# Optimization experiments

Measured on AMD Instinct MI355X. Metric: run time of the kernel, lower is better.

## Reference

```python
import jax, jax.numpy as jnp
import numpy as np

N, E = 50000, 800000
F_NODE, F_EDGE, HID, EMB, HEADS = 128, 16, 64, 32, 4
BN_EPS = 1e-5


def _glorot(key, shape):
    fan_in = shape[0] if len(shape) > 1 else shape[-1]
    return jax.random.normal(key, shape, jnp.float32) / np.sqrt(fan_in)


def setup_inputs() -> dict:
    key = jax.random.key(0)
    ks = jax.random.split(key, 32)
    inp = {
        "x": jax.random.normal(ks[0], (N, F_NODE), jnp.float32),
        "edge_attr": jax.random.normal(ks[1], (E, F_EDGE), jnp.float32),
        # GAT layer 0: in=F_NODE, heads=4, C=HID
        "W0": _glorot(ks[2], (F_NODE, HEADS * HID)),
        "We0": _glorot(ks[3], (F_EDGE, HEADS * HID)),
        "as0": _glorot(ks[4], (HEADS, HID)),
        "ad0": _glorot(ks[5], (HEADS, HID)),
        "ae0": _glorot(ks[6], (HEADS, HID)),
        "b0": jnp.zeros((HEADS * HID,), jnp.float32),
        "bn0_g": jnp.ones((HEADS * HID,), jnp.float32),
        "bn0_b": jnp.zeros((HEADS * HID,), jnp.float32),
        # GAT layer 1: in=HEADS*HID, heads=1, C=EMB
        "W1": _glorot(ks[7], (HEADS * HID, EMB)),
        "We1": _glorot(ks[8], (F_EDGE, EMB)),
        "as1": _glorot(ks[9], (1, EMB)),
        "ad1": _glorot(ks[10], (1, EMB)),
        "ae1": _glorot(ks[11], (1, EMB)),
        "b1": jnp.zeros((EMB,), jnp.float32),
        # node decoder: 32 -> 128 -> 64 -> 128
        "ndW1": _glorot(ks[12], (EMB, 2 * HID)),   "ndb1": jnp.zeros((2 * HID,), jnp.float32),
        "nd_g": jnp.ones((2 * HID,), jnp.float32), "nd_b": jnp.zeros((2 * HID,), jnp.float32),
        "ndW2": _glorot(ks[13], (2 * HID, HID)),   "ndb2": jnp.zeros((HID,), jnp.float32),
        "ndW3": _glorot(ks[14], (HID, F_NODE)),    "ndb3": jnp.zeros((F_NODE,), jnp.float32),
        # edge decoder: 2*32+16=80 -> 128 -> 64 -> 1
        "edW1": _glorot(ks[15], (2 * EMB + F_EDGE, 2 * HID)), "edb1": jnp.zeros((2 * HID,), jnp.float32),
        "ed_g": jnp.ones((2 * HID,), jnp.float32), "ed_b": jnp.zeros((2 * HID,), jnp.float32),
        "edW2": _glorot(ks[16], (2 * HID, HID)),   "edb2": jnp.zeros((HID,), jnp.float32),
        "edW3": _glorot(ks[17], (HID, 1)),         "edb3": jnp.zeros((1,), jnp.float32),
        "edge_index": jax.random.randint(ks[18], (2, E), 0, N, jnp.int64),
    }
    return inp


def _bn(x, g, b):
    # eval-mode BatchNorm1d with running mean 0, var 1
    return x / np.sqrt(1.0 + BN_EPS) * g + b


def _gat(x, edge_index, edge_attr, W, b, We, att_s, att_d, att_e, heads, C):
    n = x.shape[0]
    src, dst = edge_index[0], edge_index[1]
    e = edge_attr.shape[0]
    # add self loops; self-loop edge_attr = scatter-mean of incoming edge_attr (PyG fill_value='mean')
    esum = jax.ops.segment_sum(edge_attr, dst, num_segments=n)
    cnt = jax.ops.segment_sum(jnp.ones((e,), edge_attr.dtype), dst, num_segments=n)
    loop_attr = esum / jnp.maximum(cnt, 1.0)[:, None]
    loop = jnp.arange(n, dtype=src.dtype)
    src_f = jnp.concatenate([src, loop])
    dst_f = jnp.concatenate([dst, loop])
    ea = jnp.concatenate([edge_attr, loop_attr], axis=0)
    xw = (x @ W).reshape(n, heads, C)                       # [N,H,C]
    a_s = (xw * att_s).sum(-1)                              # [N,H]
    a_d = (xw * att_d).sum(-1)
    a_e = ((ea @ We).reshape(-1, heads, C) * att_e).sum(-1)  # [E+N,H]
    alpha = jax.nn.leaky_relu(a_s[src_f] + a_d[dst_f] + a_e, 0.2)
    # segment softmax over destination neighborhoods
    m = jax.ops.segment_max(alpha, dst_f, num_segments=n)
    alpha = jnp.exp(alpha - m[dst_f])
    s = jax.ops.segment_sum(alpha, dst_f, num_segments=n)
    alpha = alpha / (s[dst_f] + 1e-16)
    out = jax.ops.segment_sum(alpha[:, :, None] * xw[src_f], dst_f, num_segments=n)
    return out.reshape(n, heads * C) + b


def reference(x, edge_attr, W0, b0, We0, as0, ad0, ae0, bn0_g, bn0_b,
              W1, b1, We1, as1, ad1, ae1,
              ndW1, ndb1, nd_g, nd_b, ndW2, ndb2, ndW3, ndb3,
              edW1, edb1, ed_g, ed_b, edW2, edb2, edW3, edb3,
              edge_index):
    # encoder
    h = _gat(x, edge_index, edge_attr, W0, b0, We0, as0, ad0, ae0, HEADS, HID)
    h = jax.nn.elu(_bn(h, bn0_g, bn0_b))  # residual skipped: 256 != 128; dropout is eval-mode identity
    z = _gat(h, edge_index, edge_attr, W1, b1, We1, as1, ad1, ae1, 1, EMB)
    # node decoder
    n1 = _bn(jax.nn.relu(z @ ndW1 + ndb1), nd_g, nd_b)
    node_recon = jax.nn.relu(n1 @ ndW2 + ndb2) @ ndW3 + ndb3
    # edge decoder
    src, dst = edge_index[0], edge_index[1]
    ef = jnp.concatenate([z[src], z[dst], edge_attr], axis=1)  # [E, 2*EMB+F_EDGE]
    e1 = _bn(jax.nn.relu(ef @ edW1 + edb1), ed_g, ed_b)
    edge_recon = jax.nn.sigmoid((jax.nn.relu(e1 @ edW2 + edb2) @ edW3 + edb3)).squeeze(-1)
    return (z, node_recon, edge_recon)
```

## Files before the change

### kernel.cpp

```cpp
#include <hip/hip_runtime.h>
#include <math.h>

#define BN_K 0.9999950000374997f

static __device__ __forceinline__ float lrelu02(float x) { return x > 0.f ? x : 0.2f * x; }

typedef _Float16 half8 __attribute__((ext_vector_type(8)));
typedef __fp16 fp16x2 __attribute__((ext_vector_type(2)));
typedef float f32x4 __attribute__((ext_vector_type(4)));

static __device__ __forceinline__ unsigned short f2h(float x)
{
    union { _Float16 h; unsigned short u; } q;
    q.h = (_Float16)x;
    return q.u;
}
static __device__ __forceinline__ float h2f(unsigned short u)
{
    union { unsigned short u; _Float16 h; } q;
    q.u = u;
    return (float)q.h;
}
static __device__ __forceinline__ unsigned pkrtz(float a, float b)
{
    union { fp16x2 h; unsigned u; } q;
    q.h = __builtin_amdgcn_cvt_pkrtz(a, b);
    return q.u;
}

__global__ void k_ae_vec(const float* __restrict__ We0, const float* __restrict__ ae0,
                         const float* __restrict__ We1, const float* __restrict__ ae1,
                         const float* __restrict__ edbb, const float* __restrict__ edW2,
                         const float* __restrict__ edb2,
                         float* __restrict__ v0, float* __restrict__ v1,
                         float* __restrict__ b2p)
{
    int t = threadIdx.x;
    if (t < 64) {
        int h = t >> 4, k = t & 15;
        float s = 0.f;
        for (int c = 0; c < 64; ++c) s += We0[k * 256 + h * 64 + c] * ae0[h * 64 + c];
        v0[h * 16 + k] = s;
    } else if (t < 80) {
        int k = t - 64;
        float s = 0.f;
        for (int c = 0; c < 32; ++c) s += We1[k * 32 + c] * ae1[c];
        v1[k] = s;
    } else if (t < 144) {
        int n = t - 80;
        float s = 0.f;
        for (int k = 0; k < 128; ++k) s += edbb[k] * edW2[k * 64 + n];
        b2p[n] = edb2[n] + s;
    }
}

__global__ void k_deg_init(int* __restrict__ deg, int N)
{
    int i = blockIdx.x * blockDim.x + threadIdx.x;
    if (i < N) deg[i] = 1;
}

__global__ void k_deg_count(const int* __restrict__ dst, int* __restrict__ deg, int E)
{
    int e = blockIdx.x * blockDim.x + threadIdx.x;
    if (e < E) atomicAdd(&deg[dst[e]], 1);
}

#define SCHUNK 4096
__global__ __launch_bounds__(1024) void k_scan1(const int* __restrict__ deg,
                                                int* __restrict__ rowptr,
                                                int* __restrict__ bsum, int n)
{
    __shared__ int sbuf[1024];
    int b = blockIdx.x, t = threadIdx.x;
    int i0 = b * SCHUNK + t * 4;
    int v[4];
#pragma unroll
    for (int j = 0; j < 4; ++j) v[j] = (i0 + j < n) ? deg[i0 + j] : 0;
    int s = v[0] + v[1] + v[2] + v[3];
    sbuf[t] = s;
    __syncthreads();
    for (int d = 1; d < 1024; d <<= 1) {
        int tmp = (t >= d) ? sbuf[t - d] : 0;
        __syncthreads();
        sbuf[t] += tmp;
        __syncthreads();
    }
    int run = sbuf[t] - s;
#pragma unroll
    for (int j = 0; j < 4; ++j) {
        run += v[j];
        if (i0 + j < n) rowptr[i0 + j + 1] = run;
    }
    if (t == 1023) bsum[b] = sbuf[1023];
    if (b == 0 && t == 0) rowptr[0] = 0;
}

__global__ void k_scan3(const int* __restrict__ bsum, const int* __restrict__ deg,
                        int* __restrict__ rowptr, int* __restrict__ cur, int n)
{
    int i = blockIdx.x * blockDim.x + threadIdx.x;
    if (i >= n) return;
    int chunk = i / SCHUNK;
    int off = 0;
    for (int b = 0; b < chunk; ++b) off += bsum[b];
    int r = rowptr[i + 1] + off;
    rowptr[i + 1] = r;
    cur[i] = r - deg[i];
}

__global__ void k_fill(const int* __restrict__ dst, int* __restrict__ cur,
                       int* __restrict__ col, int E, int N)
{
    int t = blockIdx.x * blockDim.x + threadIdx.x;
    if (t >= E + N) return;
    int d = (t < E) ? dst[t] : (t - E);
    int slot = atomicAdd(&cur[d], 1);
    col[slot] = t;
}

__global__ __launch_bounds__(256) void k_loop_mean(
    const int* __restrict__ rowptr, const int* __restrict__ col,
    const float* __restrict__ ea, const float* __restrict__ v0, const float* __restrict__ v1,
    float* __restrict__ a_e0, float* __restrict__ a_e1, int N, int E)
{
    int wv = threadIdx.x >> 6, lane = threadIdx.x & 63;
    int i = blockIdx.x * 4 + wv;
    if (i >= N) return;
    int beg = rowptr[i], end = rowptr[i + 1];
    int q = lane >> 4, k = lane & 15;
    float sum = 0.f;
    for (int p = beg + q; p < end; p += 4) {
        int eid = col[p];
        if (eid < E) sum += ea[(size_t)eid * 16 + k];
    }
    sum += __shfl_xor(sum, 16);
    sum += __shfl_xor(sum, 32);
    int cnt = end - beg - 1;
    float mean = sum / (float)max(cnt, 1);
    float p0 = mean * v0[q * 16 + k];
    float p1 = mean * v1[k];
#pragma unroll
    for (int mm = 1; mm < 16; mm <<= 1) { p0 += __shfl_xor(p0, mm); p1 += __shfl_xor(p1, mm); }
    if (k == 0) a_e0[(size_t)(E + i) * 4 + q] = p0;
    if (lane == 0) a_e1[E + i] = p1;
}

__global__ void k_edge_ae(const float* __restrict__ ea,
                          const float* __restrict__ v0, const float* __restrict__ v1,
                          float* __restrict__ a_e0, float* __restrict__ a_e1,
                          unsigned short* __restrict__ ea16, int E)
{
    int idx = blockIdx.x * blockDim.x + threadIdx.x;
    if (idx >= E) return;
    const float* row = ea + (size_t)idx * 16;
    float r[16];
#pragma unroll
    for (int k = 0; k < 16; ++k) r[k] = row[k];
#pragma unroll
    for (int h = 0; h < 4; ++h) {
        float s = 0.f;
#pragma unroll
        for (int k = 0; k < 16; ++k) s = fmaf(r[k], v0[h * 16 + k], s);
        a_e0[(size_t)idx * 4 + h] = s;
    }
    float s1 = 0.f;
#pragma unroll
    for (int k = 0; k < 16; ++k) s1 = fmaf(r[k], v1[k], s1);
    a_e1[idx] = s1;
#pragma unroll
    for (int k = 0; k < 16; k += 4) {
        ushort4 o;
        o.x = f2h(r[k]); o.y = f2h(r[k + 1]); o.z = f2h(r[k + 2]); o.w = f2h(r[k + 3]);
        *(ushort4*)(ea16 + (size_t)idx * 16 + k) = o;
    }
}

__global__ __launch_bounds__(512) void k_pack_all(
    const float* __restrict__ W0, const float* __restrict__ W1,
    const float* __restrict__ nd1, const float* __restrict__ nd2, const float* __restrict__ nd3,
    const float* __restrict__ ed1, const float* __restrict__ ed2,
    const float* __restrict__ edb1, const float* __restrict__ edg,
    unsigned short* __restrict__ pw)
{
    int f = blockIdx.x, t = threadIdx.x;
    int l = t >> 3, i = t & 7, g = l >> 4, m = l & 15;
    float v;
    if (f < 64) {
        int q = f; int k = 32 * (q >> 4) + 8 * g + i, n = 16 * (q & 15) + m;
        v = W0[(size_t)k * 256 + n];
    } else if (f < 80) {
        int q = f - 64; int k = 32 * (q >> 1) + 8 * g + i, n = 16 * (q & 1) + m;
        v = W1[(size_t)k * 32 + n];
    } else if (f < 88) {
        int q = f - 80; int k = 8 * g + i, n = 16 * q + m;
        v = nd1[(size_t)k * 128 + n];
    } else if (f < 104) {
        int q = f - 88; int k = 32 * (q >> 2) + 8 * g + i, n = 16 * (q & 3) + m;
        v = nd2[(size_t)k * 64 + n];
    } else if (f < 120) {
        int q = f - 104; int k = 32 * (q >> 3) + 8 * g + i, n = 16 * (q & 7) + m;
        v = nd3[(size_t)k * 128 + n];
    } else if (f < 144) {
        int q = f - 120; int k = 32 * (q >> 3) + 8 * g + i, n = 16 * (q & 7) + m;
        v = (k < 80) ? ed1[(size_t)k * 128 + n] : (k == 80 ? edb1[n] : 0.f);
    } else {
        int q = f - 144; int k = 32 * (q >> 2) + 8 * g + i, n = 16 * (q & 3) + m;
        v = ed2[(size_t)k * 64 + n] * (edg[k] * BN_K);
    }
    pw[(size_t)f * 512 + t] = f2h(v);
}

template <int KC, int NT, int MODE, int AF32, int NTOT, int DOTS>
__global__ __launch_bounds__(256) void k_gemm16(
    const void* __restrict__ Ain, const unsigned short* __restrict__ pwB,
    void* __restrict__ outp, int M,
    const float* __restrict__ bias, const float* __restrict__ g_,
    const float* __restrict__ bb_,
    const float* __restrict__ attS, const float* __restrict__ attD,
    float* __restrict__ a_sO, float* __restrict__ a_dO)
{
    constexpr int K = KC * 32;
    constexpr int LDA = K + 8;
    __shared__ unsigned short s_pw[KC * NT * 512];
    __shared__ unsigned short s_a[64 * LDA];
    __shared__ float s_c[3 * NT * 16];

    int t = threadIdx.x;
    int ttoff = blockIdx.y * NT;
    for (int idx = t; idx < KC * NT * 64; idx += 256) {
        int f = idx >> 6, e8 = idx & 63;
        int c = f / NT, tt = f - c * NT;
        *(half8*)&s_pw[(size_t)idx * 8] =
            *(const half8*)&pwB[(((size_t)(c * NTOT + ttoff + tt)) * 64 + e8) * 8];
    }
    if (MODE) {
        for (int c = t; c < NT * 16; c += 256) {
            s_c[c] = bias[ttoff * 16 + c];
            if (MODE == 2) {
                s_c[NT * 16 + c] = g_[ttoff * 16 + c] * BN_K;
                s_c[2 * NT * 16 + c] = bb_[ttoff * 16 + c];
            }
        }
    }
    int wv = t >> 6, lane = t & 63, gq = lane >> 4, m = lane & 15;

    float asv[NT], adv[NT];
    if (DOTS) {
#pragma unroll
        for (int tt = 0; tt < NT; ++tt) {
            asv[tt] = attS[ttoff * 16 + 16 * tt + m];
            adv[tt] = attD[ttoff * 16 + 16 * tt + m];
        }
    }

    int nrt = (M + 63) >> 6;
    for (int rt = blockIdx.x; rt < nrt; rt += gridDim.x) {
        int r0 = rt << 6;
        __syncthreads();
        for (int idx = t; idx < 64 * (K / 8); idx += 256) {
            int row = idx / (K / 8), cb = idx % (K / 8);
            half8 v = {};
            if (r0 + row < M) {
                if (AF32) {
                    const float* Af = (const float*)Ain + (size_t)(r0 + row) * K + cb * 8;
                    float4 u0 = *(const float4*)Af;
                    float4 u1 = *(const float4*)(Af + 4);
                    union { half8 h; unsigned u[4]; } q;
                    q.u[0] = pkrtz(u0.x, u0.y); q.u[1] = pkrtz(u0.z, u0.w);
                    q.u[2] = pkrtz(u1.x, u1.y); q.u[3] = pkrtz(u1.z, u1.w);
                    v = q.h;
                } else {
                    v = *(const half8*)&((const unsigned short*)Ain)[(size_t)(r0 + row) * K + cb * 8];
                }
            }
            *(half8*)&s_a[row * LDA + cb * 8] = v;
        }
        __syncthreads();
        f32x4 acc[NT] = {};
#pragma unroll
        for (int c = 0; c < KC; ++c) {
            half8 a = *(half8*)&s_a[(wv * 16 + m) * LDA + 32 * c + 8 * gq];
#pragma unroll
            for (int tt = 0; tt < NT; ++tt) {
                half8 b = *(const half8*)&s_pw[(c * NT + tt) * 512 + lane * 8];
                acc[tt] = __builtin_amdgcn_mfma_f32_16x16x32_f16(a, b, acc[tt], 0, 0, 0);
            }
        }
#pragma unroll
        for (int tt = 0; tt < NT; ++tt) {
            int col = 16 * tt + m;
            int ocol = ttoff * 16 + col;
            float cb = MODE ? s_c[col] : 0.f;
#pragma unroll
            for (int r = 0; r < 4; ++r) {
                int row = r0 + wv * 16 + 4 * gq + r;
                float v = acc[tt][r] + cb;
                if (MODE == 1) v = fmaxf(v, 0.f);
                if (MODE == 2) v = fmaxf(v, 0.f) * s_c[NT * 16 + col] + s_c[2 * NT * 16 + col];
                if (MODE == 3) {
                    if (row < M) ((float*)outp)[(size_t)row * (NTOT * 16) + ocol] = v;
                } else {
                    float o = __shfl_xor(v, 1);
                    if (!(m & 1) && row < M)
                        *(unsigned*)&((unsigned short*)outp)[(size_t)row * (NTOT * 16) + ocol] =
                            pkrtz(v, o);
                }
            }
        }
        if (DOTS == 1) {
#pragma unroll
            for (int r = 0; r < 4; ++r) {
                float psA = 0.f, pdA = 0.f, psB = 0.f, pdB = 0.f;
#pragma unroll
                for (int tt = 0; tt < NT && tt < 4; ++tt) {
                    psA = fmaf(acc[tt][r], asv[tt], psA);
                    pdA = fmaf(acc[tt][r], adv[tt], pdA);
                }
#pragma unroll
                for (int tt = 4; tt < NT; ++tt) {
                    psB = fmaf(acc[tt][r], asv[tt], psB);
                    pdB = fmaf(acc[tt][r], adv[tt], pdB);
                }
#pragma unroll
                for (int mm = 1; mm < 16; mm <<= 1) {
                    psA += __shfl_xor(psA, mm); pdA += __shfl_xor(pdA, mm);
                    psB += __shfl_xor(psB, mm); pdB += __shfl_xor(pdB, mm);
                }
                int row = r0 + wv * 16 + 4 * gq + r;
                if (m == 0 && row < M) {
                    int hA = 2 * blockIdx.y;
                    a_sO[(size_t)row * 4 + hA] = psA; a_sO[(size_t)row * 4 + hA + 1] = psB;
                    a_dO[(size_t)row * 4 + hA] = pdA; a_dO[(size_t)row * 4 + hA + 1] = pdB;
                }
            }
        } else if (DOTS == 2) {
#pragma unroll
            for (int r = 0; r < 4; ++r) {
                float ps = 0.f, pd = 0.f;
#pragma unroll
                for (int tt = 0; tt < NT; ++tt) {
                    ps = fmaf(acc[tt][r], asv[tt], ps);
                    pd = fmaf(acc[tt][r], adv[tt], pd);
                }
#pragma unroll
                for (int mm = 1; mm < 16; mm <<= 1) {
                    ps += __shfl_xor(ps, mm); pd += __shfl_xor(pd, mm);
                }
                int row = r0 + wv * 16 + 4 * gq + r;
                if (m == 0 && row < M) { a_sO[row] = ps; a_dO[row] = pd; }
            }
        }
    }
}

__global__ __launch_bounds__(64) void k_gat0_agg(
    const int* __restrict__ rowptr, const int* __restrict__ col, const int* __restrict__ srcA,
    const float* __restrict__ a_s, const float* __restrict__ a_d, const float* __restrict__ a_e,
    const unsigned short* __restrict__ xw16, const float* __restrict__ b0,
    const float* __restrict__ bng, const float* __restrict__ bnb,
    unsigned short* __restrict__ hout16, int N, int E)
{
    int i = blockIdx.x;
    int lane = threadIdx.x;
    int beg = rowptr[i], end = rowptr[i + 1];
    float ad[4];
#pragma unroll
    for (int h = 0; h < 4; ++h) ad[h] = a_d[(size_t)i * 4 + h];

    float al[4] = {-1e30f, -1e30f, -1e30f, -1e30f};
    int sl0 = i;
    int p0 = beg + lane;
    if (p0 < end) {
        int eid = col[p0];
        sl0 = (eid < E) ? srcA[eid] : i;
        float4 as4 = *(const float4*)(a_s + (size_t)sl0 * 4);
        float4 ae4 = *(const float4*)(a_e + (size_t)eid * 4);
        al[0] = lrelu02(as4.x + ad[0] + ae4.x);
        al[1] = lrelu02(as4.y + ad[1] + ae4.y);
        al[2] = lrelu02(as4.z + ad[2] + ae4.z);
        al[3] = lrelu02(as4.w + ad[3] + ae4.w);
    }
    float mx[4] = {al[0], al[1], al[2], al[3]};
    for (int p = p0 + 64; p < end; p += 64) {
        int eid = col[p];
        int s = (eid < E) ? srcA[eid] : i;
        float4 as4 = *(const float4*)(a_s + (size_t)s * 4);
        float4 ae4 = *(const float4*)(a_e + (size_t)eid * 4);
        mx[0] = fmaxf(mx[0], lrelu02(as4.x + ad[0] + ae4.x));
        mx[1] = fmaxf(mx[1], lrelu02(as4.y + ad[1] + ae4.y));
        mx[2] = fmaxf(mx[2], lrelu02(as4.z + ad[2] + ae4.z));
        mx[3] = fmaxf(mx[3], lrelu02(as4.w + ad[3] + ae4.w));
    }
#pragma unroll
    for (int h = 0; h < 4; ++h)
#pragma unroll
        for (int m = 1; m < 64; m <<= 1) mx[h] = fmaxf(mx[h], __shfl_xor(mx[h], m));

    __shared__ float wls[256];
    __shared__ int s_src[64];
    int hl = lane >> 4;
    float accx = 0.f, accy = 0.f, accz = 0.f, accw = 0.f;
    float s0 = 0.f, s1 = 0.f, s2 = 0.f, s3 = 0.f;
    for (int base = beg; base < end; base += 64) {
        int p = base + lane;
        int cnt = min(64, end - base);
        if (p < end) {
            float aa0, aa1, aa2, aa3;
            int s;
            if (base == beg) {
                s = sl0;
                aa0 = al[0]; aa1 = al[1]; aa2 = al[2]; aa3 = al[3];
            } else {
                int eid = col[p];
                s = (eid < E) ? srcA[eid] : i;
                float4 as4 = *(const float4*)(a_s + (size_t)s * 4);
                float4 ae4 = *(const float4*)(a_e + (size_t)eid * 4);
                aa0 = lrelu02(as4.x + ad[0] + ae4.x);
                aa1 = lrelu02(as4.y + ad[1] + ae4.y);
                aa2 = lrelu02(as4.z + ad[2] + ae4.z);
                aa3 = lrelu02(as4.w + ad[3] + ae4.w);
            }
            float w0 = expf(aa0 - mx[0]);
            float w1 = expf(aa1 - mx[1]);
            float w2 = expf(aa2 - mx[2]);
            float w3 = expf(aa3 - mx[3]);
            s0 += w0; s1 += w1; s2 += w2; s3 += w3;
            wls[lane * 4 + 0] = w0; wls[lane * 4 + 1] = w1;
            wls[lane * 4 + 2] = w2; wls[lane * 4 + 3] = w3;
            s_src[lane] = s;
        }
        __syncthreads();
        int q = 0;
        for (; q + 3 < cnt; q += 4) {
            int ss0 = s_src[q], ss1 = s_src[q + 1], ss2 = s_src[q + 2], ss3 = s_src[q + 3];
            ushort4 x0 = *(const ushort4*)(xw16 + (size_t)ss0 * 256 + lane * 4);
            ushort4 x1 = *(const ushort4*)(xw16 + (size_t)ss1 * 256 + lane * 4);
            ushort4 x2 = *(const ushort4*)(xw16 + (size_t)ss2 * 256 + lane * 4);
            ushort4 x3 = *(const ushort4*)(xw16 + (size_t)ss3 * 256 + lane * 4);
            float w0 = wls[q * 4 + hl], w1 = wls[(q + 1) * 4 + hl];
            float w2 = wls[(q + 2) * 4 + hl], w3 = wls[(q + 3) * 4 + hl];
            accx = fmaf(w0, h2f(x0.x), accx); accy = fmaf(w0, h2f(x0.y), accy);
            accz = fmaf(w0, h2f(x0.z), accz); accw = fmaf(w0, h2f(x0.w), accw);
            accx = fmaf(w1, h2f(x1.x), accx); accy = fmaf(w1, h2f(x1.y), accy);
            accz = fmaf(w1, h2f(x1.z), accz); accw = fmaf(w1, h2f(x1.w), accw);
            accx = fmaf(w2, h2f(x2.x), accx); accy = fmaf(w2, h2f(x2.y), accy);
            accz = fmaf(w2, h2f(x2.z), accz); accw = fmaf(w2, h2f(x2.w), accw);
            accx = fmaf(w3, h2f(x3.x), accx); accy = fmaf(w3, h2f(x3.y), accy);
            accz = fmaf(w3, h2f(x3.z), accz); accw = fmaf(w3, h2f(x3.w), accw);
        }
        for (; q < cnt; ++q) {
            int ss = s_src[q];
            float w = wls[q * 4 + hl];
            ushort4 xv = *(const ushort4*)(xw16 + (size_t)ss * 256 + lane * 4);
            accx = fmaf(w, h2f(xv.x), accx);
            accy = fmaf(w, h2f(xv.y), accy);
            accz = fmaf(w, h2f(xv.z), accz);
            accw = fmaf(w, h2f(xv.w), accw);
        }
        __syncthreads();
    }
#pragma unroll
    for (int m = 1; m < 64; m <<= 1) {
        s0 += __shfl_xor(s0, m); s1 += __shfl_xor(s1, m);
        s2 += __shfl_xor(s2, m); s3 += __shfl_xor(s3, m);
    }
    float sden = ((hl == 0) ? s0 : (hl == 1) ? s1 : (hl == 2) ? s2 : s3) + 1e-16f;

    int ch = lane * 4;
    float out[4] = {accx / sden, accy / sden, accz / sden, accw / sden};
    ushort4 ov;
    unsigned short* po = (unsigned short*)&ov;
#pragma unroll
    for (int j = 0; j < 4; ++j) {
        int c = ch + j;
        float v = out[j] + b0[c];
        v = v * (BN_K * bng[c]) + bnb[c];
        po[j] = f2h((v > 0.f) ? v : expm1f(v));
    }
    *(ushort4*)(hout16 + (size_t)i * 256 + ch) = ov;
}

__global__ __launch_bounds__(64) void k_gat1_agg(
    const int* __restrict__ rowptr, const int* __restrict__ col, const int* __restrict__ srcA,
    const float* __restrict__ a_s, const float* __restrict__ a_d, const float* __restrict__ a_e,
    const unsigned short* __restrict__ xw16, const float* __restrict__ b1,
    float* __restrict__ zout, unsigned short* __restrict__ z16, int N, int E)
{
    int i = blockIdx.x;
    int lane = threadIdx.x;
    int beg = rowptr[i], end = rowptr[i + 1];
    float ad = a_d[i];
    float al = -1e30f;
    int sl0 = i;
    int p0 = beg + lane;
    if (p0 < end) {
        int eid = col[p0];
        sl0 = (eid < E) ? srcA[eid] : i;
        al = lrelu02(a_s[sl0] + ad + a_e[eid]);
    }
    float mx = al;
    for (int p = p0 + 64; p < end; p += 64) {
        int eid = col[p];
        int s = (eid < E) ? srcA[eid] : i;
        mx = fmaxf(mx, lrelu02(a_s[s] + ad + a_e[eid]));
    }
#pragma unroll
    for (int m = 1; m < 64; m <<= 1) mx = fmaxf(mx, __shfl_xor(mx, m));

    __shared__ float wls[64];
    __shared__ int s_src[64];
    float acc = 0.f, ssum = 0.f;
    int parity = lane >> 5, j = lane & 31;
    for (int base = beg; base < end; base += 64) {
        int p = base + lane;
        int cnt = min(64, end - base);
        if (p < end) {
            float aa;
            int s;
            if (base == beg) { s = sl0; aa = al; }
            else {
                int eid = col[p];
                s = (eid < E) ? srcA[eid] : i;
                aa = lrelu02(a_s[s] + ad + a_e[eid]);
            }
            float w = expf(aa - mx);
            ssum += w;
            wls[lane] = w;
            s_src[lane] = s;
        }
        __syncthreads();
        int q = parity;
        for (; q + 6 < cnt; q += 8) {
            int ss0 = s_src[q], ss1 = s_src[q + 2], ss2 = s_src[q + 4], ss3 = s_src[q + 6];
            float x0 = h2f(xw16[(size_t)ss0 * 32 + j]);
            float x1 = h2f(xw16[(size_t)ss1 * 32 + j]);
            float x2 = h2f(xw16[(size_t)ss2 * 32 + j]);
            float x3 = h2f(xw16[(size_t)ss3 * 32 + j]);
            acc = fmaf(wls[q], x0, acc);
            acc = fmaf(wls[q + 2], x1, acc);
            acc = fmaf(wls[q + 4], x2, acc);
            acc = fmaf(wls[q + 6], x3, acc);
        }
        for (; q < cnt; q += 2) {
            int ss = s_src[q];
            acc = fmaf(wls[q], h2f(xw16[(size_t)ss * 32 + j]), acc);
        }
        __syncthreads();
    }
#pragma unroll
    for (int m = 1; m < 64; m <<= 1) ssum += __shfl_xor(ssum, m);
    acc += __shfl_xor(acc, 32);
    if (lane < 32) {
        float v = acc / (ssum + 1e-16f) + b1[lane];
        zout[(size_t)i * 32 + lane] = v;
        z16[(size_t)i * 32 + lane] = f2h(v);
    }
}

#define H1_STRIDE 136

__global__ __launch_bounds__(256, 3) void k_edge_dec_mfma(
    const unsigned short* __restrict__ z16, const unsigned short* __restrict__ ea16,
    const int* __restrict__ srcA, const int* __restrict__ dstA,
    const unsigned short* __restrict__ pw,
    const float* __restrict__ b2p, const float* __restrict__ w3,
    const float* __restrict__ b3v, float* __restrict__ out, int E)
{
    __shared__ unsigned short s_pw[24 * 512];
    __shared__ unsigned short s_h1[4][16 * H1_STRIDE];

    int t = threadIdx.x;
    for (int idx = t; idx < 1536; idx += 256)
        *(half8*)&s_pw[idx * 8] = *(const half8*)&pw[idx * 8];
    __syncthreads();

    int wv = t >> 6, lane = t & 63;
    int g = lane >> 4, m = lane & 15;
    unsigned short* h1 = s_h1[wv];

    half8 w2r[16];
#pragma unroll
    for (int q = 0; q < 16; ++q)
        w2r[q] = *(const half8*)&pw[(size_t)(24 + q) * 512 + lane * 8];

    float w3t[4], b2t[4];
#pragma unroll
    for (int q = 0; q < 4; ++q) { w3t[q] = w3[16 * q + m]; b2t[q] = b2p[16 * q + m]; }
    float b3 = b3v[0];

    int ntiles = (E + 15) >> 4;
    int gw = blockIdx.x * 4 + wv;
    int nw = gridDim.x * 4;

    half8 a0n = {}, a1n = {}, a2n = {};
    {
        int e = (gw << 4) + m;
        if (gw < ntiles && e < E) {
            int si = srcA[e], di = dstA[e];
            a0n = *(const half8*)&z16[(size_t)si * 32 + 8 * g];
            a1n = *(const half8*)&z16[(size_t)di * 32 + 8 * g];
            if (g < 2) a2n = *(const half8*)&ea16[(size_t)e * 16 + 8 * g];
        }
        if (g == 2) a2n[0] = (_Float16)1.f;
    }

    for (int tile = gw; tile < ntiles; ) {
        half8 a0 = a0n, a1 = a1n, a2 = a2n;
        int e0 = tile << 4;
        int nxt = tile + nw;

        a0n = half8{}; a1n = half8{}; a2n = half8{};
        {
            int e = (nxt << 4) + m;
            if (nxt < ntiles && e < E) {
                int si = srcA[e], di = dstA[e];
                a0n = *(const half8*)&z16[(size_t)si * 32 + 8 * g];
                a1n = *(const half8*)&z16[(size_t)di * 32 + 8 * g];
                if (g < 2) a2n = *(const half8*)&ea16[(size_t)e * 16 + 8 * g];
            }
            if (g == 2) a2n[0] = (_Float16)1.f;
        }

        f32x4 acc1[8] = {};
#pragma unroll
        for (int tt = 0; tt < 8; ++tt)
            acc1[tt] = __builtin_amdgcn_mfma_f32_16x16x32_f16(a0, *(const half8*)&s_pw[(0 * 8 + tt) * 512 + lane * 8], acc1[tt], 0, 0, 0);
#pragma unroll
        for (int tt = 0; tt < 8; ++tt)
            acc1[tt] = __builtin_amdgcn_mfma_f32_16x16x32_f16(a1, *(const half8*)&s_pw[(1 * 8 + tt) * 512 + lane * 8], acc1[tt], 0, 0, 0);
#pragma unroll
        for (int tt = 0; tt < 8; ++tt)
            acc1[tt] = __builtin_amdgcn_mfma_f32_16x16x32_f16(a2, *(const half8*)&s_pw[(2 * 8 + tt) * 512 + lane * 8], acc1[tt], 0, 0, 0);

#pragma unroll
        for (int tt = 0; tt < 8; ++tt) {
#pragma unroll
            for (int r = 0; r < 4; ++r) {
                float v = fmaxf(acc1[tt][r], 0.f);
                float vo = __shfl_xor(v, 1);
                if (!(m & 1))
                    *(unsigned*)&h1[(4 * g + r) * H1_STRIDE + 16 * tt + m] = pkrtz(v, vo);
            }
        }
        asm volatile("s_waitcnt lgkmcnt(0)" ::: "memory");
        __builtin_amdgcn_sched_barrier(0);

        f32x4 acc2[4] = {};
#pragma unroll
        for (int c = 0; c < 4; ++c) {
            half8 a = *(half8*)&h1[m * H1_STRIDE + 32 * c + 8 * g];
#pragma unroll
            for (int tt = 0; tt < 4; ++tt)
                acc2[tt] = __builtin_amdgcn_mfma_f32_16x16x32_f16(a, w2r[c * 4 + tt], acc2[tt], 0, 0, 0);
        }
        float s[4];
#pragma unroll
        for (int r = 0; r < 4; ++r) {
            float acc = 0.f;
#pragma unroll
            for (int tt = 0; tt < 4; ++tt) {
                float v = fmaxf(acc2[tt][r] + b2t[tt], 0.f);
                acc = fmaf(v, w3t[tt], acc);
            }
            acc += __shfl_xor(acc, 1);
            acc += __shfl_xor(acc, 2);
            acc += __shfl_xor(acc, 4);
            acc += __shfl_xor(acc, 8);
            s[r] = acc;
        }
        if (m == 0) {
            int eb = e0 + 4 * g;
            if (eb + 3 < E) {
                float4 o;
                o.x = 1.f / (1.f + expf(-(s[0] + b3)));
                o.y = 1.f / (1.f + expf(-(s[1] + b3)));
                o.z = 1.f / (1.f + expf(-(s[2] + b3)));
                o.w = 1.f / (1.f + expf(-(s[3] + b3)));
                *(float4*)(out + eb) = o;
            } else {
#pragma unroll
                for (int r = 0; r < 4; ++r)
                    if (eb + r < E) out[eb + r] = 1.f / (1.f + expf(-(s[r] + b3)));
            }
        }
        tile = nxt;
    }
}

extern "C" void kernel_launch(void* const* d_in, const int* in_sizes, int n_in,
                              void* d_out, int out_size, void* d_ws, size_t ws_size,
                              hipStream_t stream)
{
    const float* x    = (const float*)d_in[0];
    const float* ea   = (const float*)d_in[1];
    const float* W0   = (const float*)d_in[2];
    const float* We0  = (const float*)d_in[3];
    const float* as0  = (const float*)d_in[4];
    const float* ad0  = (const float*)d_in[5];
    const float* ae0  = (const float*)d_in[6];
    const float* b0   = (const float*)d_in[7];
    const float* bn0g = (const float*)d_in[8];
    const float* bn0b = (const float*)d_in[9];
    const float* W1   = (const float*)d_in[10];
    const float* We1  = (const float*)d_in[11];
    const float* as1  = (const float*)d_in[12];
    const float* ad1  = (const float*)d_in[13];
    const float* ae1  = (const float*)d_in[14];
    const float* b1   = (const float*)d_in[15];
    const float* ndW1 = (const float*)d_in[16];
    const float* ndb1 = (const float*)d_in[17];
    const float* ndg  = (const float*)d_in[18];
    const float* ndbb = (const float*)d_in[19];
    const float* ndW2 = (const float*)d_in[20];
    const float* ndb2 = (const float*)d_in[21];
    const float* ndW3 = (const float*)d_in[22];
    const float* ndb3 = (const float*)d_in[23];
    const float* edW1 = (const float*)d_in[24];
    const float* edb1 = (const float*)d_in[25];
    const float* edg  = (const float*)d_in[26];
    const float* edbb = (const float*)d_in[27];
    const float* edW2 = (const float*)d_in[28];
    const float* edb2 = (const float*)d_in[29];
    const float* edW3 = (const float*)d_in[30];
    const float* edb3 = (const float*)d_in[31];
    const int*   eidx = (const int*)d_in[32];

    const int N = in_sizes[0] / 128;
    const int E = in_sizes[1] / 16;
    const int* srcA = eidx;
    const int* dstA = eidx + E;

    char* ws = (char*)d_ws;
    size_t o = 0;
    auto alloc = [&](size_t bytes) -> void* {
        void* p = ws + o;
        o = (o + bytes + 255) & ~(size_t)255;
        return p;
    };
    typedef unsigned short u16;
    u16*   xw0_16 = (u16*)alloc((size_t)N * 256 * 2);
    u16*   hbuf16 = (u16*)alloc((size_t)N * 256 * 2);
    u16*   xw1_16 = (u16*)alloc((size_t)N * 32 * 2);
    u16*   z16    = (u16*)alloc((size_t)N * 32 * 2);
    u16*   n1_16  = (u16*)alloc((size_t)N * 128 * 2);
    u16*   h2n16  = (u16*)alloc((size_t)N * 64 * 2);
    u16*   ea16   = (u16*)alloc((size_t)E * 16 * 2);
    float* a_s0   = (float*)alloc((size_t)N * 4 * 4);
    float* a_d0   = (float*)alloc((size_t)N * 4 * 4);
    float* a_e0a  = (float*)alloc((size_t)(E + N) * 4 * 4);
    float* a_e1a  = (float*)alloc((size_t)(E + N) * 4);
    float* a_s1   = (float*)alloc((size_t)N * 4);
    float* a_d1   = (float*)alloc((size_t)N * 4);
    int*   deg    = (int*)alloc((size_t)N * 4);
    int*   rowptr = (int*)alloc((size_t)(N + 1) * 4);
    int*   cur    = (int*)alloc((size_t)N * 4);
    int*   col    = (int*)alloc((size_t)(E + N) * 4);
    int*   bsum   = (int*)alloc(64 * 4);
    float* v0     = (float*)alloc(64 * 4);
    float* v1     = (float*)alloc(16 * 4);
    float* b2p    = (float*)alloc(64 * 4);
    u16*   pw     = (u16*)alloc((size_t)160 * 512 * 2);

    float* z_out    = (float*)d_out;
    float* node_out = z_out + (size_t)N * 32;
    float* edge_out = node_out + (size_t)N * 128;

    const int nb = (N + SCHUNK - 1) / SCHUNK;
    const int nrt = (N + 63) / 64;

    k_pack_all<<<160, 512, 0, stream>>>(W0, W1, ndW1, ndW2, ndW3, edW1, edW2, edb1, edg, pw);
    k_ae_vec<<<1, 192, 0, stream>>>(We0, ae0, We1, ae1, edbb, edW2, edb2, v0, v1, b2p);
    k_deg_init<<<(N + 255) / 256, 256, 0, stream>>>(deg, N);
    k_deg_count<<<(E + 255) / 256, 256, 0, stream>>>(dstA, deg, E);
    k_scan1<<<nb, 1024, 0, stream>>>(deg, rowptr, bsum, N);
    k_scan3<<<(N + 255) / 256, 256, 0, stream>>>(bsum, deg, rowptr, cur, N);
    k_fill<<<(E + N + 255) / 256, 256, 0, stream>>>(dstA, cur, col, E, N);
    k_loop_mean<<<(N + 3) / 4, 256, 0, stream>>>(rowptr, col, ea, v0, v1, a_e0a, a_e1a, N, E);
    k_edge_ae<<<(E + 255) / 256, 256, 0, stream>>>(ea, v0, v1, a_e0a, a_e1a, ea16, E);

    k_gemm16<4, 8, 0, 1, 16, 1><<<dim3(nrt, 2), 256, 0, stream>>>(
        x, pw, xw0_16, N, nullptr, nullptr, nullptr, as0, ad0, a_s0, a_d0);
    k_gat0_agg<<<N, 64, 0, stream>>>(rowptr, col, srcA, a_s0, a_d0, a_e0a, xw0_16, b0, bn0g, bn0b,
                                     hbuf16, N, E);

    k_gemm16<8, 2, 0, 0, 2, 2><<<dim3(nrt, 1), 256, 0, stream>>>(
        hbuf16, pw + (size_t)64 * 512, xw1_16, N, nullptr, nullptr, nullptr,
        as1, ad1, a_s1, a_d1);
    k_gat1_agg<<<N, 64, 0, stream>>>(rowptr, col, srcA, a_s1, a_d1, a_e1a, xw1_16, b1,
                                     z_out, z16, N, E);

    k_gemm16<1, 8, 2, 0, 8, 0><<<dim3(nrt, 1), 256, 0, stream>>>(
        z16, pw + (size_t)80 * 512, n1_16, N, ndb1, ndg, ndbb, nullptr, nullptr, nullptr, nullptr);
    k_gemm16<4, 4, 1, 0, 4, 0><<<dim3(nrt, 1), 256, 0, stream>>>(
        n1_16, pw + (size_t)88 * 512, h2n16, N, ndb2, nullptr, nullptr, nullptr, nullptr, nullptr, nullptr);
    k_gemm16<2, 8, 3, 0, 8, 0><<<dim3(nrt, 1), 256, 0, stream>>>(
        h2n16, pw + (size_t)104 * 512, node_out, N, ndb3, nullptr, nullptr, nullptr, nullptr, nullptr, nullptr);

    k_edge_dec_mfma<<<768, 256, 0, stream>>>(z16, ea16, srcA, dstA, pw + (size_t)120 * 512,
                                             b2p, edW3, edb3, edge_out, E);
}
```

Measured before the change: 424.5 us.

## Use two waves per node in GAT0 aggregation and read fp16 edge attrs in loop mean

The layer-0 attention aggregation now runs 128 threads per node instead of 64. Each thread handles two channels, and the per-wave softmax max and sum are combined through shared memory. This is meant to raise parallelism and memory-level concurrency on the gather-heavy aggregation, at the cost of extra barriers and narrower per-thread loads. Separately, the self-loop mean kernel now runs after the edge kernel so it can read the fp16 copy of the edge attributes, halving its gather bytes but adding fp16 rounding to the mean.

```diff
diff --git a/kernel.cpp b/kernel.cpp
--- a/kernel.cpp
+++ b/kernel.cpp
@@ -121,7 +121,8 @@
 
 __global__ __launch_bounds__(256) void k_loop_mean(
     const int* __restrict__ rowptr, const int* __restrict__ col,
-    const float* __restrict__ ea, const float* __restrict__ v0, const float* __restrict__ v1,
+    const unsigned short* __restrict__ ea16,
+    const float* __restrict__ v0, const float* __restrict__ v1,
     float* __restrict__ a_e0, float* __restrict__ a_e1, int N, int E)
 {
     int wv = threadIdx.x >> 6, lane = threadIdx.x & 63;
@@ -132,7 +133,7 @@
     float sum = 0.f;
     for (int p = beg + q; p < end; p += 4) {
         int eid = col[p];
-        if (eid < E) sum += ea[(size_t)eid * 16 + k];
+        if (eid < E) sum += h2f(ea16[(size_t)eid * 16 + k]);
     }
     sum += __shfl_xor(sum, 16);
     sum += __shfl_xor(sum, 32);
@@ -354,7 +355,7 @@
     }
 }
 
-__global__ __launch_bounds__(64) void k_gat0_agg(
+__global__ __launch_bounds__(128) void k_gat0_agg(
     const int* __restrict__ rowptr, const int* __restrict__ col, const int* __restrict__ srcA,
     const float* __restrict__ a_s, const float* __restrict__ a_d, const float* __restrict__ a_e,
     const unsigned short* __restrict__ xw16, const float* __restrict__ b0,
@@ -362,7 +363,8 @@
     unsigned short* __restrict__ hout16, int N, int E)
 {
     int i = blockIdx.x;
-    int lane = threadIdx.x;
+    int tid = threadIdx.x;
+    int wv = tid >> 6, lane = tid & 63;
     int beg = rowptr[i], end = rowptr[i + 1];
     float ad[4];
 #pragma unroll
@@ -370,7 +372,7 @@
 
     float al[4] = {-1e30f, -1e30f, -1e30f, -1e30f};
     int sl0 = i;
-    int p0 = beg + lane;
+    int p0 = beg + tid;
     if (p0 < end) {
         int eid = col[p0];
         sl0 = (eid < E) ? srcA[eid] : i;
@@ -382,7 +384,7 @@
         al[3] = lrelu02(as4.w + ad[3] + ae4.w);
     }
     float mx[4] = {al[0], al[1], al[2], al[3]};
-    for (int p = p0 + 64; p < end; p += 64) {
+    for (int p = p0 + 128; p < end; p += 128) {
         int eid = col[p];
         int s = (eid < E) ? srcA[eid] : i;
         float4 as4 = *(const float4*)(a_s + (size_t)s * 4);
@@ -397,14 +399,26 @@
 #pragma unroll
         for (int m = 1; m < 64; m <<= 1) mx[h] = fmaxf(mx[h], __shfl_xor(mx[h], m));
 
-    __shared__ float wls[256];
-    __shared__ int s_src[64];
-    int hl = lane >> 4;
-    float accx = 0.f, accy = 0.f, accz = 0.f, accw = 0.f;
+    __shared__ float s_mx[2][4];
+    __shared__ float s_part[2][4];
+    if (lane == 0) {
+#pragma unroll
+        for (int h = 0; h < 4; ++h) s_mx[wv][h] = mx[h];
+    }
+    __syncthreads();
+    float mxf[4];
+#pragma unroll
+    for (int h = 0; h < 4; ++h) mxf[h] = fmaxf(s_mx[0][h], s_mx[1][h]);
+
+    __shared__ float wls[128 * 4];
+    __shared__ int s_src[128];
+    int ch = wv * 128 + lane * 2;
+    int hl = ch >> 6;
+    float accA = 0.f, accB = 0.f;
     float s0 = 0.f, s1 = 0.f, s2 = 0.f, s3 = 0.f;
-    for (int base = beg; base < end; base += 64) {
-        int p = base + lane;
-        int cnt = min(64, end - base);
+    for (int base = beg; base < end; base += 128) {
+        int p = base + tid;
+        int cnt = min(128, end - base);
         if (p < end) {
             float aa0, aa1, aa2, aa3;
             int s;
@@ -421,42 +435,36 @@
                 aa2 = lrelu02(as4.z + ad[2] + ae4.z);
                 aa3 = lrelu02(as4.w + ad[3] + ae4.w);
             }
-            float w0 = expf(aa0 - mx[0]);
-            float w1 = expf(aa1 - mx[1]);
-            float w2 = expf(aa2 - mx[2]);
-            float w3 = expf(aa3 - mx[3]);
+            float w0 = expf(aa0 - mxf[0]);
+            float w1 = expf(aa1 - mxf[1]);
+            float w2 = expf(aa2 - mxf[2]);
+            float w3 = expf(aa3 - mxf[3]);
             s0 += w0; s1 += w1; s2 += w2; s3 += w3;
-            wls[lane * 4 + 0] = w0; wls[lane * 4 + 1] = w1;
-            wls[lane * 4 + 2] = w2; wls[lane * 4 + 3] = w3;
-            s_src[lane] = s;
+            wls[tid * 4 + 0] = w0; wls[tid * 4 + 1] = w1;
+            wls[tid * 4 + 2] = w2; wls[tid * 4 + 3] = w3;
+            s_src[tid] = s;
         }
         __syncthreads();
         int q = 0;
         for (; q + 3 < cnt; q += 4) {
             int ss0 = s_src[q], ss1 = s_src[q + 1], ss2 = s_src[q + 2], ss3 = s_src[q + 3];
-            ushort4 x0 = *(const ushort4*)(xw16 + (size_t)ss0 * 256 + lane * 4);
-            ushort4 x1 = *(const ushort4*)(xw16 + (size_t)ss1 * 256 + lane * 4);
-            ushort4 x2 = *(const ushort4*)(xw16 + (size_t)ss2 * 256 + lane * 4);
-            ushort4 x3 = *(const ushort4*)(xw16 + (size_t)ss3 * 256 + lane * 4);
             float w0 = wls[q * 4 + hl], w1 = wls[(q + 1) * 4 + hl];
             float w2 = wls[(q + 2) * 4 + hl], w3 = wls[(q + 3) * 4 + hl];
-            accx = fmaf(w0, h2f(x0.x), accx); accy = fmaf(w0, h2f(x0.y), accy);
-            accz = fmaf(w0, h2f(x0.z), accz); accw = fmaf(w0, h2f(x0.w), accw);
-            accx = fmaf(w1, h2f(x1.x), accx); accy = fmaf(w1, h2f(x1.y), accy);
-            accz = fmaf(w1, h2f(x1.z), accz); accw = fmaf(w1, h2f(x1.w), accw);
-            accx = fmaf(w2, h2f(x2.x), accx); accy = fmaf(w2, h2f(x2.y), accy);
-            accz = fmaf(w2, h2f(x2.z), accz); accw = fmaf(w2, h2f(x2.w), accw);
-            accx = fmaf(w3, h2f(x3.x), accx); accy = fmaf(w3, h2f(x3.y), accy);
-            accz = fmaf(w3, h2f(x3.z), accz); accw = fmaf(w3, h2f(x3.w), accw);
+            ushort2 x0 = *(const ushort2*)(xw16 + (size_t)ss0 * 256 + ch);
+            ushort2 x1 = *(const ushort2*)(xw16 + (size_t)ss1 * 256 + ch);
+            ushort2 x2 = *(const ushort2*)(xw16 + (size_t)ss2 * 256 + ch);
+            ushort2 x3 = *(const ushort2*)(xw16 + (size_t)ss3 * 256 + ch);
+            accA = fmaf(w0, h2f(x0.x), accA); accB = fmaf(w0, h2f(x0.y), accB);
+            accA = fmaf(w1, h2f(x1.x), accA); accB = fmaf(w1, h2f(x1.y), accB);
+            accA = fmaf(w2, h2f(x2.x), accA); accB = fmaf(w2, h2f(x2.y), accB);
+            accA = fmaf(w3, h2f(x3.x), accA); accB = fmaf(w3, h2f(x3.y), accB);
         }
         for (; q < cnt; ++q) {
             int ss = s_src[q];
             float w = wls[q * 4 + hl];
-            ushort4 xv = *(const ushort4*)(xw16 + (size_t)ss * 256 + lane * 4);
-            accx = fmaf(w, h2f(xv.x), accx);
-            accy = fmaf(w, h2f(xv.y), accy);
-            accz = fmaf(w, h2f(xv.z), accz);
-            accw = fmaf(w, h2f(xv.w), accw);
+            ushort2 xv = *(const ushort2*)(xw16 + (size_t)ss * 256 + ch);
+            accA = fmaf(w, h2f(xv.x), accA);
+            accB = fmaf(w, h2f(xv.y), accB);
         }
         __syncthreads();
     }
@@ -465,20 +473,20 @@
         s0 += __shfl_xor(s0, m); s1 += __shfl_xor(s1, m);
         s2 += __shfl_xor(s2, m); s3 += __shfl_xor(s3, m);
     }
-    float sden = ((hl == 0) ? s0 : (hl == 1) ? s1 : (hl == 2) ? s2 : s3) + 1e-16f;
-
-    int ch = lane * 4;
-    float out[4] = {accx / sden, accy / sden, accz / sden, accw / sden};
-    ushort4 ov;
-    unsigned short* po = (unsigned short*)&ov;
-#pragma unroll
-    for (int j = 0; j < 4; ++j) {
-        int c = ch + j;
-        float v = out[j] + b0[c];
-        v = v * (BN_K * bng[c]) + bnb[c];
-        po[j] = f2h((v > 0.f) ? v : expm1f(v));
-    }
-    *(ushort4*)(hout16 + (size_t)i * 256 + ch) = ov;
+    if (lane == 0) {
+        s_part[wv][0] = s0; s_part[wv][1] = s1; s_part[wv][2] = s2; s_part[wv][3] = s3;
+    }
+    __syncthreads();
+    float sden = s_part[0][hl] + s_part[1][hl] + 1e-16f;
+
+    float o0 = accA / sden + b0[ch];
+    float o1 = accB / sden + b0[ch + 1];
+    o0 = o0 * (BN_K * bng[ch]) + bnb[ch];
+    o1 = o1 * (BN_K * bng[ch + 1]) + bnb[ch + 1];
+    ushort2 ov;
+    ov.x = f2h((o0 > 0.f) ? o0 : expm1f(o0));
+    ov.y = f2h((o1 > 0.f) ? o1 : expm1f(o1));
+    *(ushort2*)(hout16 + (size_t)i * 256 + ch) = ov;
 }
 
 __global__ __launch_bounds__(64) void k_gat1_agg(
@@ -776,13 +784,13 @@
     k_scan1<<<nb, 1024, 0, stream>>>(deg, rowptr, bsum, N);
     k_scan3<<<(N + 255) / 256, 256, 0, stream>>>(bsum, deg, rowptr, cur, N);
     k_fill<<<(E + N + 255) / 256, 256, 0, stream>>>(dstA, cur, col, E, N);
-    k_loop_mean<<<(N + 3) / 4, 256, 0, stream>>>(rowptr, col, ea, v0, v1, a_e0a, a_e1a, N, E);
     k_edge_ae<<<(E + 255) / 256, 256, 0, stream>>>(ea, v0, v1, a_e0a, a_e1a, ea16, E);
+    k_loop_mean<<<(N + 3) / 4, 256, 0, stream>>>(rowptr, col, ea16, v0, v1, a_e0a, a_e1a, N, E);
 
     k_gemm16<4, 8, 0, 1, 16, 1><<<dim3(nrt, 2), 256, 0, stream>>>(
         x, pw, xw0_16, N, nullptr, nullptr, nullptr, as0, ad0, a_s0, a_d0);
-    k_gat0_agg<<<N, 64, 0, stream>>>(rowptr, col, srcA, a_s0, a_d0, a_e0a, xw0_16, b0, bn0g, bn0b,
-                                     hbuf16, N, E);
+    k_gat0_agg<<<N, 128, 0, stream>>>(rowptr, col, srcA, a_s0, a_d0, a_e0a, xw0_16, b0, bn0g, bn0b,
+                                      hbuf16, N, E);
 
     k_gemm16<8, 2, 0, 0, 2, 2><<<dim3(nrt, 1), 256, 0, stream>>>(
         hbuf16, pw + (size_t)64 * 512, xw1_16, N, nullptr, nullptr, nullptr,
```

New measurement: 430.3 us. Within noise of the previous version (+1.4%).
